# Performance work log

Measured on AMD Instinct MI355X. Metric: run time of the kernel, lower is better.

The kernel has to match this reference:

```python
import jax, jax.numpy as jnp
import numpy as np
import math

B, LQ, D = 4, 1024, 2048
H, G = 16, 4            # n_heads, n_groups
HD = D // H             # 128
GS = H // G             # group_size = 4
PAST = 1024
LK = PAST + LQ
NEG = jnp.float32(-1e30)


def _rope(x, cos, sin):
    # x: [B, L, nh, HD]; cos/sin: [1, L, 1, HD//2]; llama-style complex rotation
    x1 = x[..., 0::2]
    x2 = x[..., 1::2]
    r1 = x1 * cos - x2 * sin
    r2 = x1 * sin + x2 * cos
    return jnp.stack([r1, r2], axis=-1).reshape(x.shape)


def setup_inputs() -> dict:
    key = jax.random.key(0)
    ks = jax.random.split(key, 12)
    s = 0.02
    x = jax.random.normal(ks[0], (B, LQ, D), jnp.float32)
    past_k = jax.random.normal(ks[1], (B, G, PAST, HD), jnp.float32)
    past_v = jax.random.normal(ks[2], (B, G, PAST, HD), jnp.float32)
    rotary_freqs = jax.random.uniform(ks[3], (LQ, HD // 2), jnp.float32) * 6.283
    # causal mask with cache: query i may attend to key j if j <= PAST + i
    q_pos = PAST + jnp.arange(LQ)[:, None]
    k_pos = jnp.arange(LK)[None, :]
    mask = (k_pos <= q_pos)  # [LQ, LK] bool
    Wq = jax.random.normal(ks[4], (D, D), jnp.float32) * s
    bq = jnp.zeros((D,), jnp.float32)
    Wk = jax.random.normal(ks[5], (D, G * HD), jnp.float32) * s
    bk = jnp.zeros((G * HD,), jnp.float32)
    Wv = jax.random.normal(ks[6], (D, G * HD), jnp.float32) * s
    bv = jnp.zeros((G * HD,), jnp.float32)
    Wo = jax.random.normal(ks[7], (D, D), jnp.float32) * s
    bo = jnp.zeros((D,), jnp.float32)
    return {"x": x, "mask": mask, "rotary_freqs": rotary_freqs,
            "past_k": past_k, "past_v": past_v,
            "Wq": Wq, "bq": bq, "Wk": Wk, "bk": bk,
            "Wv": Wv, "bv": bv, "Wo": Wo, "bo": bo}


def reference(x, mask, rotary_freqs, past_k, past_v, Wq, bq, Wk, bk, Wv, bv, Wo, bo):
    # projections (torch Linear math with weights stored [in, out])
    q = (x @ Wq + bq).reshape(B, LQ, H, HD)      # break_heads: [B,L,H,HD]
    k = (x @ Wk + bk).reshape(B, LQ, G, HD)      # [B,L,G,HD]
    v = (x @ Wv + bv).reshape(B, LQ, G, HD).transpose(0, 2, 1, 3)  # [B,G,L,HD]
    # RoPE on q,k then move heads forward (matches q.transpose(2,1))
    cos = jnp.cos(rotary_freqs)[None, :, None, :]
    sin = jnp.sin(rotary_freqs)[None, :, None, :]
    q = _rope(q, cos, sin).transpose(0, 2, 1, 3)  # [B,H,LQ,HD]
    k = _rope(k, cos, sin).transpose(0, 2, 1, 3)  # [B,G,LQ,HD]
    # KV cache append
    k = jnp.concatenate([past_k, k], axis=2)      # [B,G,LK,HD]
    v = jnp.concatenate([past_v, v], axis=2)
    # grouped-query attention
    qg = q.reshape(B, G, GS, LQ, HD)
    scores = jnp.einsum('bgsqd,bgkd->bgsqk', qg, k) / math.sqrt(HD)
    scores = jnp.where(mask[None, None, None, :, :], scores, NEG)
    att = jax.nn.softmax(scores, axis=-1)
    out = jnp.einsum('bgsqk,bgkd->bgsqd', att, v).reshape(B, H, LQ, HD)
    out = out.transpose(0, 2, 1, 3).reshape(B, LQ, D)  # concatenate_heads
    return out @ Wo + bo
```

## Files before the change

### kernel.cpp

```cpp
#include <hip/hip_runtime.h>

#define B_   4
#define LQ_  1024
#define D_   2048
#define H_   16
#define G_   4
#define HD_  128
#define GS_  4
#define PAST_ 1024
#define LK_  2048
#define NQKV 3072

typedef __attribute__((ext_vector_type(8))) short short8;
typedef __attribute__((ext_vector_type(4))) float f32x4;

__device__ __forceinline__ ushort f2b(float f) {
    unsigned u = __builtin_bit_cast(unsigned, f);
    u += 0x7FFF + ((u >> 16) & 1);
    return (ushort)(u >> 16);
}
__device__ __forceinline__ float b2f(ushort h) {
    unsigned u = ((unsigned)h) << 16;
    return __builtin_bit_cast(float, u);
}

#define GLD_LDS16(gp, lp) \
    __builtin_amdgcn_global_load_lds((__attribute__((address_space(1))) void*)(gp), \
                                     (__attribute__((address_space(3))) void*)(lp), 16, 0, 0)

__global__ __launch_bounds__(256) void prep_misc(const float* __restrict__ x,
                                                 ushort* __restrict__ xb,
                                                 const float* __restrict__ pk,
                                                 ushort* __restrict__ kc,
                                                 const float* __restrict__ bq,
                                                 const float* __restrict__ bk,
                                                 const float* __restrict__ bv,
                                                 float* __restrict__ bias) {
    int blk = blockIdx.x;
    int tid = threadIdx.x;
    if (blk < 8192) {
        int i = blk * 256 + tid;
        float4 v = ((const float4*)x)[i];
        ushort4 o;
        o.x = f2b(v.x); o.y = f2b(v.y); o.z = f2b(v.z); o.w = f2b(v.w);
        ((ushort4*)xb)[i] = o;
    } else if (blk < 10240) {
        int i = (blk - 8192) * 256 + tid;
        float4 v = ((const float4*)pk)[i];
        int bg  = i >> 15;
        int rem = i & 32767;
        ushort4 o;
        o.x = f2b(v.x); o.y = f2b(v.y); o.z = f2b(v.z); o.w = f2b(v.w);
        ((ushort4*)kc)[(size_t)bg * 65536 + rem] = o;
    } else {
        int i = (blk - 10240) * 256 + tid;
        if (i < 2048) bias[i] = bq[i];
        else if (i < 2560) bias[i] = bk[i - 2048];
        else if (i < 3072) bias[i] = bv[i - 2560];
    }
}

__global__ __launch_bounds__(256) void transpose_pack(const float* __restrict__ in,
                                                      ushort* __restrict__ out,
                                                      int rows_in, int cols_in,
                                                      long in_bstride, long out_bstride,
                                                      int out_rstride) {
    __shared__ float t[32][33];
    int bz = blockIdx.z;
    in  += (long)bz * in_bstride;
    out += (long)bz * out_bstride;
    int c0 = blockIdx.x * 32, r0 = blockIdx.y * 32;
    int tx = threadIdx.x, ty = threadIdx.y;
    #pragma unroll
    for (int i = 0; i < 32; i += 8) {
        int r = r0 + ty + i;
        if (r < rows_in && (c0 + tx) < cols_in)
            t[ty + i][tx] = in[(long)r * cols_in + c0 + tx];
    }
    __syncthreads();
    #pragma unroll
    for (int i = 0; i < 32; i += 8) {
        int c = c0 + ty + i, r = r0 + tx;
        if (c < cols_in && r < rows_in)
            out[(long)c * out_rstride + r] = f2b(t[tx][ty + i]);
    }
}

template <bool BF16_OUT>
__global__ __launch_bounds__(256) void gemm_bt(const ushort* __restrict__ A,
                                               const ushort* __restrict__ Bt,
                                               const float* __restrict__ bias,
                                               void* __restrict__ Cout,
                                               int M, int N, int K) {
    __shared__ ushort lA[128 * 32];
    __shared__ ushort lB[128 * 32];
    const int tid = threadIdx.x;
    const int wave = tid >> 6, lane = tid & 63;
    const int quad = lane >> 4, l15 = lane & 15;
    const int m0 = blockIdx.y * 128, n0 = blockIdx.x * 128;
    const int wm = (wave >> 1) * 64, wn = (wave & 1) * 64;

    f32x4 acc[4][4];
    #pragma unroll
    for (int i = 0; i < 4; ++i)
        #pragma unroll
        for (int j = 0; j < 4; ++j)
            #pragma unroll
            for (int r = 0; r < 4; ++r) acc[i][j][r] = 0.f;

    for (int k0 = 0; k0 < K; k0 += 32) {
        __syncthreads();
        #pragma unroll
        for (int i = 0; i < 2; ++i) {
            int chunk = wave * 2 + i;
            int flat = chunk * 512 + lane * 8;
            int row = flat >> 5, col = flat & 31;
            GLD_LDS16(A  + (size_t)(m0 + row) * K + k0 + col, lA + chunk * 512);
            GLD_LDS16(Bt + (size_t)(n0 + row) * K + k0 + col, lB + chunk * 512);
        }
        __syncthreads();
        short8 af[4], bf[4];
        #pragma unroll
        for (int i = 0; i < 4; ++i)
            af[i] = *(const short8*)(lA + (wm + i * 16 + l15) * 32 + quad * 8);
        #pragma unroll
        for (int j = 0; j < 4; ++j)
            bf[j] = *(const short8*)(lB + (wn + j * 16 + l15) * 32 + quad * 8);
        #pragma unroll
        for (int i = 0; i < 4; ++i)
            #pragma unroll
            for (int j = 0; j < 4; ++j)
                acc[i][j] = __builtin_amdgcn_mfma_f32_16x16x32_bf16(af[i], bf[j], acc[i][j], 0, 0, 0);
    }

    #pragma unroll
    for (int i = 0; i < 4; ++i)
        #pragma unroll
        for (int j = 0; j < 4; ++j)
            #pragma unroll
            for (int r = 0; r < 4; ++r) {
                int row = m0 + wm + i * 16 + quad * 4 + r;
                int col = n0 + wn + j * 16 + l15;
                float v = acc[i][j][r] + bias[col];
                if (BF16_OUT) ((ushort*)Cout)[(size_t)row * N + col] = f2b(v);
                else          ((float*)Cout)[(size_t)row * N + col] = v;
            }
}

__global__ __launch_bounds__(256) void rope_pack(const ushort* __restrict__ qkvb,
                                                 const float* __restrict__ rf,
                                                 ushort* __restrict__ qb,
                                                 ushort* __restrict__ kc,
                                                 ushort* __restrict__ vtc) {
    const float SC = 0.08838834764831845f;
    int row = blockIdx.x;
    int b = row >> 10, qi = row & 1023;
    int tid = threadIdx.x;
    const ushort* src = qkvb + (size_t)row * NQKV;

    for (int p = tid; p < 1024; p += 256) {
        int h = p >> 6, i = p & 63;
        float fr = rf[qi * 64 + i];
        float s, c; __sincosf(fr, &s, &c);
        uint pr = *(const uint*)(src + h * 128 + 2 * i);
        float x1 = b2f((ushort)(pr & 0xffff));
        float x2 = b2f((ushort)(pr >> 16));
        float r1 = (x1 * c - x2 * s) * SC;
        float r2 = (x1 * s + x2 * c) * SC;
        size_t o = (((size_t)(b * H_ + h)) * LQ_ + qi) * HD_ + 2 * i;
        *(uint*)(qb + o) = (uint)f2b(r1) | ((uint)f2b(r2) << 16);
    }
    {
        int g = tid >> 6, i = tid & 63;
        float fr = rf[qi * 64 + i];
        float s, c; __sincosf(fr, &s, &c);
        uint pr = *(const uint*)(src + 2048 + g * 128 + 2 * i);
        float x1 = b2f((ushort)(pr & 0xffff));
        float x2 = b2f((ushort)(pr >> 16));
        float r1 = x1 * c - x2 * s;
        float r2 = x1 * s + x2 * c;
        size_t o = (((size_t)(b * G_ + g)) * LK_ + PAST_ + qi) * HD_ + 2 * i;
        *(uint*)(kc + o) = (uint)f2b(r1) | ((uint)f2b(r2) << 16);
    }
    for (int e = tid; e < 512; e += 256) {
        int g = e >> 7, d = e & 127;
        vtc[(((size_t)(b * G_ + g)) * HD_ + d) * LK_ + PAST_ + qi] = src[2560 + e];
    }
}

__global__ __launch_bounds__(256, 2) void attn_kernel(const ushort* __restrict__ qb,
                                                      const ushort* __restrict__ kc,
                                                      const ushort* __restrict__ vtc,
                                                      ushort* __restrict__ attn_a) {
    __shared__ ushort kt[2][64 * 128];
    __shared__ ushort vtt[2][128 * 64];
    __shared__ ushort pt[128 * 64];

    const int tid = threadIdx.x;
    const int wave = tid >> 6, lane = tid & 63;
    const int quad = lane >> 4, l15 = lane & 15;
    const int qh = wave >> 1;
    const int jw = wave & 1;
    const int tile = (blockIdx.y < 32) ? blockIdx.x : (7 - (int)blockIdx.x);
    const int q0 = tile << 7;
    const int bh = blockIdx.y;
    const int b = bh >> 4, h = bh & 15, g = h >> 2;
    const ushort* kcb = kc + ((size_t)(b * G_ + g)) * LK_ * HD_;
    const ushort* vcb = vtc + ((size_t)(b * G_ + g)) * HD_ * LK_;

    int ksrc[4], vsrc[4];
    #pragma unroll
    for (int i = 0; i < 4; ++i) {
        int u = (wave * 4 + i) * 64 + lane;
        int key = u >> 4, cs = u & 15;
        ksrc[i] = key * HD_ + ((cs ^ (key & 15)) << 3);
        int d = u >> 3, c2 = u & 7;
        vsrc[i] = d * LK_ + ((c2 ^ (d & 7)) << 3);
    }

    short8 qf[4][4];
    #pragma unroll
    for (int qfr = 0; qfr < 4; ++qfr) {
        int qrow = q0 + qh * 64 + qfr * 16 + l15;
        const ushort* qp = qb + (((size_t)(b * H_ + h)) * LQ_ + qrow) * HD_ + quad * 8;
        #pragma unroll
        for (int kk = 0; kk < 4; ++kk) qf[qfr][kk] = *(const short8*)(qp + kk * 32);
    }

    f32x4 o[4][4];
    #pragma unroll
    for (int qfr = 0; qfr < 4; ++qfr)
        #pragma unroll
        for (int f = 0; f < 4; ++f)
            #pragma unroll
            for (int r = 0; r < 4; ++r) o[qfr][f][r] = 0.f;
    float lst[4][4];
    #pragma unroll
    for (int qfr = 0; qfr < 4; ++qfr)
        #pragma unroll
        for (int r = 0; r < 4; ++r) lst[qfr][r] = 0.f;

    const int nsteps = (PAST_ + q0 + 128) >> 6;

    #pragma unroll
    for (int i = 0; i < 4; ++i) {
        int ci = wave * 4 + i;
        GLD_LDS16(kcb + ksrc[i], kt[0] + ci * 512);
        GLD_LDS16(vcb + vsrc[i], vtt[0] + ci * 512);
    }

    for (int it = 0; it < nsteps; ++it) {
        const int k0 = it << 6;
        const int cur = it & 1, nxt = cur ^ 1;
        __syncthreads();
        if (it + 1 < nsteps) {
            const int k1 = k0 + 64;
            #pragma unroll
            for (int i = 0; i < 4; ++i) {
                int ci = wave * 4 + i;
                GLD_LDS16(kcb + (size_t)k1 * HD_ + ksrc[i], kt[nxt] + ci * 512);
                GLD_LDS16(vcb + k1 + vsrc[i], vtt[nxt] + ci * 512);
            }
        }

        f32x4 z[4][2];
        #pragma unroll
        for (int qfr = 0; qfr < 4; ++qfr)
            #pragma unroll
            for (int kf = 0; kf < 2; ++kf)
                #pragma unroll
                for (int r = 0; r < 4; ++r) z[qfr][kf][r] = 0.f;
        __builtin_amdgcn_s_setprio(1);
        #pragma unroll
        for (int kk = 0; kk < 4; ++kk) {
            #pragma unroll
            for (int kf = 0; kf < 2; ++kf) {
                int key = jw * 32 + kf * 16 + l15;
                const short8 bk = *(const short8*)(kt[cur] + key * 128 + (((kk * 4 + quad) ^ l15) << 3));
                #pragma unroll
                for (int qfr = 0; qfr < 4; ++qfr)
                    z[qfr][kf] = __builtin_amdgcn_mfma_f32_16x16x32_bf16(qf[qfr][kk], bk, z[qfr][kf], 0, 0, 0);
            }
        }
        __builtin_amdgcn_s_setprio(0);

        const bool mask_step = (it >= nsteps - 2);
        #pragma unroll
        for (int qfr = 0; qfr < 4; ++qfr) {
            #pragma unroll
            for (int kf = 0; kf < 2; ++kf) {
                #pragma unroll
                for (int r = 0; r < 4; ++r) {
                    int row = qh * 64 + qfr * 16 + quad * 4 + r;
                    int col = jw * 32 + kf * 16 + l15;
                    float pv_ = __expf(z[qfr][kf][r]);
                    if (mask_step) {
                        int qpos = PAST_ + q0 + row;
                        if (k0 + col > qpos) pv_ = 0.f;
                    }
                    lst[qfr][r] += pv_;
                    pt[row * 64 + ((((col >> 3) ^ (row & 7)) << 3) | (col & 7))] = f2b(pv_);
                }
            }
        }

        asm volatile("s_waitcnt lgkmcnt(0)" ::: "memory");
        __builtin_amdgcn_s_barrier();
        __builtin_amdgcn_sched_barrier(0);

        __builtin_amdgcn_s_setprio(1);
        #pragma unroll
        for (int j2 = 0; j2 < 2; ++j2) {
            short8 pa[4];
            #pragma unroll
            for (int qfr = 0; qfr < 4; ++qfr) {
                int prow = qh * 64 + qfr * 16 + l15;
                pa[qfr] = *(const short8*)(pt + prow * 64 + (((j2 * 4 + quad) ^ (prow & 7)) << 3));
            }
            #pragma unroll
            for (int f = 0; f < 4; ++f) {
                int d = jw * 64 + f * 16 + l15;
                const short8 bv = *(const short8*)(vtt[cur] + d * 64 + (((j2 * 4 + quad) ^ (l15 & 7)) << 3));
                #pragma unroll
                for (int qfr = 0; qfr < 4; ++qfr)
                    o[qfr][f] = __builtin_amdgcn_mfma_f32_16x16x32_bf16(pa[qfr], bv, o[qfr][f], 0, 0, 0);
            }
        }
        __builtin_amdgcn_s_setprio(0);
    }

    __syncthreads();
    float* scr = (float*)pt;
    #pragma unroll
    for (int qfr = 0; qfr < 4; ++qfr)
        #pragma unroll
        for (int r = 0; r < 4; ++r)
            scr[wave * 1024 + (qfr * 4 + r) * 64 + lane] = lst[qfr][r];
    __syncthreads();
    #pragma unroll
    for (int qfr = 0; qfr < 4; ++qfr) {
        float linv[4];
        #pragma unroll
        for (int r = 0; r < 4; ++r) {
            float rs = lst[qfr][r] + scr[(wave ^ 1) * 1024 + (qfr * 4 + r) * 64 + lane];
            rs += __shfl_xor(rs, 1);
            rs += __shfl_xor(rs, 2);
            rs += __shfl_xor(rs, 4);
            rs += __shfl_xor(rs, 8);
            linv[r] = 1.0f / rs;
        }
        #pragma unroll
        for (int f = 0; f < 4; ++f)
            #pragma unroll
            for (int r = 0; r < 4; ++r) {
                int q = q0 + qh * 64 + qfr * 16 + quad * 4 + r;
                int d = jw * 64 + f * 16 + l15;
                attn_a[((size_t)(b * LQ_ + q)) * D_ + h * HD_ + d] = f2b(o[qfr][f][r] * linv[r]);
            }
    }
}


extern "C" void kernel_launch(void* const* d_in, const int* in_sizes, int n_in,
                              void* d_out, int out_size, void* d_ws, size_t ws_size,
                              hipStream_t stream) {
    const float* x  = (const float*)d_in[0];
    const float* rf = (const float*)d_in[2];
    const float* pk = (const float*)d_in[3];
    const float* pv = (const float*)d_in[4];
    const float* Wq = (const float*)d_in[5];
    const float* bq = (const float*)d_in[6];
    const float* Wk = (const float*)d_in[7];
    const float* bk = (const float*)d_in[8];
    const float* Wv = (const float*)d_in[9];
    const float* bv = (const float*)d_in[10];
    const float* Wo = (const float*)d_in[11];
    const float* bo = (const float*)d_in[12];
    float* out = (float*)d_out;

    char* p = (char*)d_ws;
    auto take = [&](size_t n) { void* r = p; p += (n + 255) & ~(size_t)255; return r; };
    ushort* xb       = (ushort*)take((size_t)4096 * 2048 * 2);
    ushort* wt_qkv   = (ushort*)take((size_t)3072 * 2048 * 2);
    ushort* wt_o     = (ushort*)take((size_t)2048 * 2048 * 2);
    float*  bias_qkv = (float*) take((size_t)3072 * 4);
    ushort* qkvb     = (ushort*)take((size_t)4096 * 3072 * 2);
    ushort* qb       = (ushort*)take((size_t)B_ * H_ * LQ_ * HD_ * 2);
    ushort* kcache   = (ushort*)take((size_t)B_ * G_ * LK_ * HD_ * 2);
    ushort* vtc      = (ushort*)take((size_t)B_ * G_ * HD_ * LK_ * 2);
    ushort* attn_a   = (ushort*)take((size_t)4096 * 2048 * 2);

    dim3 tb(32, 8);
    prep_misc<<<10252, 256, 0, stream>>>(x, xb, pk, kcache, bq, bk, bv, bias_qkv);
    transpose_pack<<<dim3(64, 64, 1), tb, 0, stream>>>(Wq, wt_qkv, 2048, 2048, 0, 0, 2048);
    transpose_pack<<<dim3(16, 64, 1), tb, 0, stream>>>(Wk, wt_qkv + (size_t)2048 * 2048, 2048, 512, 0, 0, 2048);
    transpose_pack<<<dim3(16, 64, 1), tb, 0, stream>>>(Wv, wt_qkv + (size_t)2560 * 2048, 2048, 512, 0, 0, 2048);
    transpose_pack<<<dim3(64, 64, 1), tb, 0, stream>>>(Wo, wt_o, 2048, 2048, 0, 0, 2048);
    transpose_pack<<<dim3(4, 32, 16), tb, 0, stream>>>(pv, vtc, 1024, 128,
                                                       (long)1024 * 128, (long)128 * 2048, 2048);

    gemm_bt<true><<<dim3(24, 32), 256, 0, stream>>>(xb, wt_qkv, bias_qkv, qkvb, 4096, 3072, 2048);
    rope_pack<<<4096, 256, 0, stream>>>(qkvb, rf, qb, kcache, vtc);
    attn_kernel<<<dim3(8, 64), 256, 0, stream>>>(qb, kcache, vtc, attn_a);
    gemm_bt<false><<<dim3(16, 32), 256, 0, stream>>>(attn_a, wt_o, bo, out, 4096, 2048, 2048);
}
```

Before: 405.3 us.

## Replace GEMM with 256x256-tile, double-buffered, swizzled-LDS pipelined kernel

Replaces the 128x128, single-buffered, K=32 GEMM with a 512-thread kernel that computes 256x256 output tiles at K-step 64. Global-to-LDS loads are double-buffered and staggered across four phases, with s_setprio and barriers so loads overlap MFMA work. LDS rows use an XOR swizzle to avoid bank conflicts. The larger tile raises arithmetic intensity, but the grids shrink to 192 and 128 blocks, which may underfill the 256 CUs, and register pressure rises from 128 accumulators per thread.

```diff
diff --git a/kernel.cpp b/kernel.cpp
--- a/kernel.cpp
+++ b/kernel.cpp
@@ -87,64 +87,141 @@
 }
 
 template <bool BF16_OUT>
-__global__ __launch_bounds__(256) void gemm_bt(const ushort* __restrict__ A,
-                                               const ushort* __restrict__ Bt,
-                                               const float* __restrict__ bias,
-                                               void* __restrict__ Cout,
-                                               int M, int N, int K) {
-    __shared__ ushort lA[128 * 32];
-    __shared__ ushort lB[128 * 32];
+__global__ __launch_bounds__(512, 2) void gemm256(const ushort* __restrict__ Ap,
+                                                  const ushort* __restrict__ Bp,
+                                                  const float* __restrict__ bias,
+                                                  void* __restrict__ Cout,
+                                                  int M, int N, int K) {
+    __shared__ ushort sh[65536];
     const int tid = threadIdx.x;
-    const int wave = tid >> 6, lane = tid & 63;
+    const int w = tid >> 6, lane = tid & 63;
     const int quad = lane >> 4, l15 = lane & 15;
-    const int m0 = blockIdx.y * 128, n0 = blockIdx.x * 128;
-    const int wm = (wave >> 1) * 64, wn = (wave & 1) * 64;
-
-    f32x4 acc[4][4];
-    #pragma unroll
-    for (int i = 0; i < 4; ++i)
+    const int wr = w >> 2, wc = w & 3;
+    const int m0 = blockIdx.y * 256, n0 = blockIdx.x * 256;
+
+    const int u0 = w * 64 + lane, u1 = (8 + w) * 64 + lane;
+    const int r0_ = u0 >> 3, s0_ = u0 & 7;
+    const int r1_ = u1 >> 3, s1_ = u1 & 7;
+    const int sw0 = (s0_ ^ (r0_ & 7)) << 3, sw1 = (s1_ ^ (r1_ & 7)) << 3;
+    const int srcA00 = (m0 + r0_) * K + sw0;
+    const int srcA01 = (m0 + r1_) * K + sw1;
+    const int srcA10 = (m0 + 128 + r0_) * K + sw0;
+    const int srcA11 = (m0 + 128 + r1_) * K + sw1;
+    const int srcB00 = (n0 + r0_) * K + sw0;
+    const int srcB01 = (n0 + r1_) * K + sw1;
+    const int srcB10 = (n0 + 128 + r0_) * K + sw0;
+    const int srcB11 = (n0 + 128 + r1_) * K + sw1;
+
+#define STAGE_A0(t, bufx) do { ushort* d_ = sh + (bufx) * 32768 + w * 512; \
+    GLD_LDS16(Ap + (size_t)(srcA00 + (t) * 64), d_); \
+    GLD_LDS16(Ap + (size_t)(srcA01 + (t) * 64), d_ + 4096); } while (0)
+#define STAGE_A1(t, bufx) do { ushort* d_ = sh + (bufx) * 32768 + 8192 + w * 512; \
+    GLD_LDS16(Ap + (size_t)(srcA10 + (t) * 64), d_); \
+    GLD_LDS16(Ap + (size_t)(srcA11 + (t) * 64), d_ + 4096); } while (0)
+#define STAGE_B0(t, bufx) do { ushort* d_ = sh + (bufx) * 32768 + 16384 + w * 512; \
+    GLD_LDS16(Bp + (size_t)(srcB00 + (t) * 64), d_); \
+    GLD_LDS16(Bp + (size_t)(srcB01 + (t) * 64), d_ + 4096); } while (0)
+#define STAGE_B1(t, bufx) do { ushort* d_ = sh + (bufx) * 32768 + 16384 + 8192 + w * 512; \
+    GLD_LDS16(Bp + (size_t)(srcB10 + (t) * 64), d_); \
+    GLD_LDS16(Bp + (size_t)(srcB11 + (t) * 64), d_ + 4096); } while (0)
+
+#define READ_A(QR) \
+    _Pragma("unroll") for (int fi = 0; fi < 4; ++fi) \
+    _Pragma("unroll") for (int ks = 0; ks < 2; ++ks) \
+        a[fi * 2 + ks] = *(const short8*)(Ab + (wr * 128 + (QR) * 64 + fi * 16 + l15) * 64 + \
+                                          (((ks * 4 + quad) ^ (l15 & 7)) << 3));
+#define READ_B(QC, BREG) \
+    _Pragma("unroll") for (int fj = 0; fj < 2; ++fj) \
+    _Pragma("unroll") for (int ks = 0; ks < 2; ++ks) \
+        BREG[fj * 2 + ks] = *(const short8*)(Bb + (wc * 64 + (QC) * 32 + fj * 16 + l15) * 64 + \
+                                             (((ks * 4 + quad) ^ (l15 & 7)) << 3));
+#define MFMA_Q(QR, QC, BREG) \
+    _Pragma("unroll") for (int ks = 0; ks < 2; ++ks) \
+    _Pragma("unroll") for (int fj = 0; fj < 2; ++fj) \
+    _Pragma("unroll") for (int fi = 0; fi < 4; ++fi) \
+        acc[(QR) * 4 + fi][(QC) * 2 + fj] = __builtin_amdgcn_mfma_f32_16x16x32_bf16( \
+            a[fi * 2 + ks], BREG[fj * 2 + ks], acc[(QR) * 4 + fi][(QC) * 2 + fj], 0, 0, 0);
+
+#define PH_MID() do { asm volatile("" ::: "memory"); __builtin_amdgcn_s_barrier(); \
+    asm volatile("s_waitcnt lgkmcnt(0)" ::: "memory"); __builtin_amdgcn_sched_barrier(0); \
+    __builtin_amdgcn_s_setprio(1); } while (0)
+#define PH_END() do { __builtin_amdgcn_s_setprio(0); asm volatile("" ::: "memory"); \
+    __builtin_amdgcn_s_barrier(); asm volatile("" ::: "memory"); } while (0)
+
+    f32x4 acc[8][4];
+    #pragma unroll
+    for (int i = 0; i < 8; ++i)
         #pragma unroll
         for (int j = 0; j < 4; ++j)
             #pragma unroll
             for (int r = 0; r < 4; ++r) acc[i][j][r] = 0.f;
 
-    for (int k0 = 0; k0 < K; k0 += 32) {
-        __syncthreads();
-        #pragma unroll
-        for (int i = 0; i < 2; ++i) {
-            int chunk = wave * 2 + i;
-            int flat = chunk * 512 + lane * 8;
-            int row = flat >> 5, col = flat & 31;
-            GLD_LDS16(A  + (size_t)(m0 + row) * K + k0 + col, lA + chunk * 512);
-            GLD_LDS16(Bt + (size_t)(n0 + row) * K + k0 + col, lB + chunk * 512);
-        }
-        __syncthreads();
-        short8 af[4], bf[4];
-        #pragma unroll
-        for (int i = 0; i < 4; ++i)
-            af[i] = *(const short8*)(lA + (wm + i * 16 + l15) * 32 + quad * 8);
-        #pragma unroll
-        for (int j = 0; j < 4; ++j)
-            bf[j] = *(const short8*)(lB + (wn + j * 16 + l15) * 32 + quad * 8);
-        #pragma unroll
-        for (int i = 0; i < 4; ++i)
-            #pragma unroll
-            for (int j = 0; j < 4; ++j)
-                acc[i][j] = __builtin_amdgcn_mfma_f32_16x16x32_bf16(af[i], bf[j], acc[i][j], 0, 0, 0);
-    }
-
-    #pragma unroll
-    for (int i = 0; i < 4; ++i)
-        #pragma unroll
-        for (int j = 0; j < 4; ++j)
+    const int KT = K >> 6;
+
+    STAGE_A0(0, 0); STAGE_A1(0, 0); STAGE_B0(0, 0); STAGE_B1(0, 0);
+    STAGE_B0(1, 1); STAGE_B1(1, 1);
+    asm volatile("s_waitcnt vmcnt(4)" ::: "memory");
+    asm volatile("" ::: "memory");
+    __builtin_amdgcn_s_barrier();
+    asm volatile("" ::: "memory");
+
+    short8 a[8], b0[4], b1[4];
+    for (int t = 0; t < KT; ++t) {
+        const int buf = t & 1;
+        const ushort* Ab = sh + buf * 32768;
+        const ushort* Bb = Ab + 16384;
+
+        READ_A(0)
+        READ_B(0, b0)
+        if (t + 1 < KT) STAGE_A0(t + 1, buf ^ 1);
+        PH_MID();
+        MFMA_Q(0, 0, b0)
+        PH_END();
+
+        READ_B(1, b1)
+        if (t + 1 < KT) STAGE_A1(t + 1, buf ^ 1);
+        PH_MID();
+        MFMA_Q(0, 1, b1)
+        PH_END();
+
+        READ_A(1)
+        if (t + 2 < KT) STAGE_B0(t + 2, buf);
+        PH_MID();
+        MFMA_Q(1, 0, b0)
+        PH_END();
+
+        if (t + 2 < KT) {
+            STAGE_B1(t + 2, buf);
+            asm volatile("s_waitcnt vmcnt(4)" ::: "memory");
+        } else {
+            asm volatile("s_waitcnt vmcnt(0)" ::: "memory");
+        }
+        PH_MID();
+        MFMA_Q(1, 1, b1)
+        PH_END();
+    }
+
+    #pragma unroll
+    for (int fi = 0; fi < 8; ++fi)
+        #pragma unroll
+        for (int fj = 0; fj < 4; ++fj)
             #pragma unroll
             for (int r = 0; r < 4; ++r) {
-                int row = m0 + wm + i * 16 + quad * 4 + r;
-                int col = n0 + wn + j * 16 + l15;
-                float v = acc[i][j][r] + bias[col];
+                int row = m0 + wr * 128 + fi * 16 + quad * 4 + r;
+                int col = n0 + wc * 64 + fj * 16 + l15;
+                float v = acc[fi][fj][r] + bias[col];
                 if (BF16_OUT) ((ushort*)Cout)[(size_t)row * N + col] = f2b(v);
                 else          ((float*)Cout)[(size_t)row * N + col] = v;
             }
+#undef STAGE_A0
+#undef STAGE_A1
+#undef STAGE_B0
+#undef STAGE_B1
+#undef READ_A
+#undef READ_B
+#undef MFMA_Q
+#undef PH_MID
+#undef PH_END
 }
 
 __global__ __launch_bounds__(256) void rope_pack(const ushort* __restrict__ qkvb,
@@ -399,8 +476,8 @@
     transpose_pack<<<dim3(4, 32, 16), tb, 0, stream>>>(pv, vtc, 1024, 128,
                                                        (long)1024 * 128, (long)128 * 2048, 2048);
 
-    gemm_bt<true><<<dim3(24, 32), 256, 0, stream>>>(xb, wt_qkv, bias_qkv, qkvb, 4096, 3072, 2048);
+    gemm256<true><<<dim3(12, 16), 512, 0, stream>>>(xb, wt_qkv, bias_qkv, qkvb, 4096, 3072, 2048);
     rope_pack<<<4096, 256, 0, stream>>>(qkvb, rf, qb, kcache, vtc);
     attn_kernel<<<dim3(8, 64), 256, 0, stream>>>(qb, kcache, vtc, attn_a);
-    gemm_bt<false><<<dim3(16, 32), 256, 0, stream>>>(attn_a, wt_o, bo, out, 4096, 2048, 2048);
-}
+    gemm256<false><<<dim3(8, 16), 512, 0, stream>>>(attn_a, wt_o, bo, out, 4096, 2048, 2048);
+}
```

New measurement: 399.0 us. About the same (-1.6%).
